# Performance work log

Measured on AMD Instinct MI355X. Metric: run time of the kernel, lower is better.

The kernel has to match this reference:

```python
import math
import jax, jax.numpy as jnp
import numpy as np

B, T, S, C, E = 16, 1024, 1024, 1024, 1024
NORM_C = 0.5


def setup_inputs() -> dict:
    key = jax.random.key(0)
    ks = jax.random.split(key, 9)
    return {
        "x": jax.random.normal(ks[0], (B, T, C), dtype=jnp.float32),
        "target_embedding": jax.random.normal(ks[1], (B, T, E), dtype=jnp.float32),
        "enc_keys": jax.random.normal(ks[2], (B, E, S), dtype=jnp.float32),      # encoder_out[0]
        "enc_values": jax.random.normal(ks[3], (B, S, E), dtype=jnp.float32),    # encoder_out[1]
        "encoder_padding_mask": jax.random.randint(ks[4], (B, S), 0, 2).astype(bool),
        "w_in": jax.random.normal(ks[5], (E, C), dtype=jnp.float32) / np.sqrt(C),
        "b_in": jnp.zeros((E,), dtype=jnp.float32),
        "w_out": jax.random.normal(ks[6], (C, E), dtype=jnp.float32) / np.sqrt(E),
        "b_out": jnp.zeros((C,), dtype=jnp.float32),
    }


def reference(x, target_embedding, enc_keys, enc_values, encoder_padding_mask,
              w_in, b_in, w_out, b_out):
    scale = jnp.float32(math.sqrt(NORM_C))
    residual = x
    # in_projection + target embedding, rescale
    h = (jnp.einsum("btc,ec->bte", x, w_in) + b_in + target_embedding) * scale
    # attention scores: bmm with keys [B,E,S]
    scores = jnp.einsum("bte,bes->bts", h, enc_keys)
    neg_inf = jnp.float32(float("-inf"))
    scores = jnp.where(encoder_padding_mask[:, None, :], neg_inf, scores)
    attn_scores = jax.nn.softmax(scores, axis=-1)
    # weighted sum of values
    ctx = jnp.einsum("bts,bse->bte", attn_scores, enc_values)
    # data-dependent rescale: multiply by sqrt(valid token count)
    s = jnp.float32(S) - jnp.sum(encoder_padding_mask.astype(ctx.dtype), axis=1, keepdims=True)  # [B,1]
    s = s[:, :, None]  # [B,1,1]
    ctx = ctx * (s * jax.lax.rsqrt(s))
    out = (jnp.einsum("bte,ce->btc", ctx, w_out) + b_out + residual) * scale
    return (out, attn_scores)
```

## Files before the change

### kernel.cpp

```cpp
#include <hip/hip_runtime.h>


#define SCALE_F 0.70710678118654752440f

constexpr int BB = 16, TT = 1024, SS = 1024, CC = 1024, EE = 1024;

typedef float    f32x4 __attribute__((ext_vector_type(4)));
typedef _Float16 f16x8 __attribute__((ext_vector_type(8)));
typedef _Float16 f16x4 __attribute__((ext_vector_type(4)));

__device__ __forceinline__ void gload_lds16(const _Float16* g, _Float16* l) {
  __builtin_amdgcn_global_load_lds((const __attribute__((address_space(1))) void*)g,
                                   (__attribute__((address_space(3))) void*)l,
                                   16, 0, 0);
}

#define VMCNT(N) asm volatile("s_waitcnt vmcnt(" #N ")" ::: "memory")
#define LGKM(N)  asm volatile("s_waitcnt lgkmcnt(" #N ")" ::: "memory")
#define SBAR()   asm volatile("s_barrier" ::: "memory")
#define DSR(dst, a, off) \
  asm volatile("ds_read_b128 %0, %1 offset:" #off : "=v"(dst) : "v"(a))

__global__ __launch_bounds__(256) void cvt_f16(const float* __restrict__ s,
                                               _Float16* __restrict__ d, long n) {
  long i = ((long)blockIdx.x * 256 + threadIdx.x) * 8;
  if (i >= n) return;
  f32x4 a = *(const f32x4*)(s + i);
  f32x4 b = *(const f32x4*)(s + i + 4);
  f16x8 h;
  h[0]=(_Float16)a[0]; h[1]=(_Float16)a[1]; h[2]=(_Float16)a[2]; h[3]=(_Float16)a[3];
  h[4]=(_Float16)b[0]; h[5]=(_Float16)b[1]; h[6]=(_Float16)b[2]; h[7]=(_Float16)b[3];
  *(f16x8*)(d + i) = h;
}

__global__ __launch_bounds__(256) void transpose_cvt(const float* __restrict__ src,
                                                     _Float16* __restrict__ dst,
                                                     int R, int Cc) {
  __shared__ float tile[64][65];
  const int b = blockIdx.z;
  const int r0 = blockIdx.y * 64, c0 = blockIdx.x * 64;
  const int t = threadIdx.x;
  const int tr = t >> 4, tc4 = (t & 15) * 4;
  const float* s = src + (size_t)b * R * Cc;
#pragma unroll
  for (int i = 0; i < 4; ++i) {
    f32x4 v = *(const f32x4*)(s + (size_t)(r0 + i * 16 + tr) * Cc + c0 + tc4);
    tile[i * 16 + tr][tc4 + 0] = v[0]; tile[i * 16 + tr][tc4 + 1] = v[1];
    tile[i * 16 + tr][tc4 + 2] = v[2]; tile[i * 16 + tr][tc4 + 3] = v[3];
  }
  __syncthreads();
  _Float16* d = dst + (size_t)b * Cc * R;
#pragma unroll
  for (int j = 0; j < 4; ++j) {
    const int cl = j * 16 + tr;
    f16x4 h;
    h[0] = (_Float16)tile[tc4 + 0][cl]; h[1] = (_Float16)tile[tc4 + 1][cl];
    h[2] = (_Float16)tile[tc4 + 2][cl]; h[3] = (_Float16)tile[tc4 + 3][cl];
    *(f16x4*)(d + (size_t)(c0 + cl) * R + r0 + tc4) = h;
  }
}

__global__ __launch_bounds__(256) void mask_prep(const unsigned char* __restrict__ mraw,
                                                 float* __restrict__ maskneg,
                                                 float* __restrict__ sscale) {
  const int b = blockIdx.x, t = threadIdx.x;
  __shared__ int bytemode_sh, cnt_sh;
  if (t == 0) { bytemode_sh = 0; cnt_sh = 0; }
  __syncthreads();
  const unsigned int* mu = (const unsigned int*)mraw;
  int local = 0;
  for (int i = t; i < (BB * SS) / 4; i += 256) {
    unsigned int v = mu[i];
    if (v != 0u && v != 1u && v != 0x3f800000u) local = 1;
  }
  if (local) atomicOr(&bytemode_sh, 1);
  __syncthreads();
  const int bytemode = bytemode_sh;
  int cnt = 0;
  for (int s = t; s < SS; s += 256) {
    int m = bytemode ? (mraw[b * SS + s] != 0) : (mu[b * SS + s] != 0u);
    maskneg[b * SS + s] = m ? -__builtin_inff() : 0.0f;
    cnt += m;
  }
#pragma unroll
  for (int o = 32; o; o >>= 1) cnt += __shfl_down(cnt, o);
  if ((t & 63) == 0) atomicAdd(&cnt_sh, cnt);
  __syncthreads();
  if (t == 0) {
    float sv = (float)SS - (float)cnt_sh;
    sscale[b] = sv * rsqrtf(sv);
  }
}

template <int EPI>
__global__ __launch_bounds__(512, 2)
void gemm_t3(const _Float16* __restrict__ A, const _Float16* __restrict__ Bmat,
             long aStride, long bStride, long oStride,
             int M, int N, int K,
             void* __restrict__ outp,
             const float* __restrict__ bias,
             const void* __restrict__ addmat,
             const float* __restrict__ extra) {
  __shared__ __attribute__((aligned(16))) _Float16 smem[73728];

  const int t = threadIdx.x;
  const int lane = t & 63;
  const int wid = t >> 6;
  const int wm = wid >> 1, wn = wid & 1;
  const int z = blockIdx.z;
  const int lo = lane & 15, hi = lane >> 4;
  const int nt = K >> 6;

  const int gx = gridDim.x;
  const int fblk = blockIdx.x + blockIdx.y * gx;
  const int q = (gx * gridDim.y) >> 3;
  const int wg = (fblk & 7) * q + (fblk >> 3);
  const long rowBase = (long)(wg / gx) * 256;
  const long colBase = (long)(wg % gx) * 128;

  const _Float16* Ag = A + (size_t)z * aStride + rowBase * K;
  const _Float16* Bg = Bmat + (size_t)z * bStride + colBase * K;

  const int strow = t >> 2;
  const int stchunk = (t & 3) ^ ((t >> 3) & 3);

  f32x4 acc[4][4] = {};

  auto stg6 = [&](int U, int b3) {
    _Float16* ab = &smem[b3 * 16384];
    _Float16* bb = &smem[49152 + b3 * 8192];
    const size_t ko = (size_t)U * 64 + stchunk * 8;
    gload_lds16(Ag + (size_t)strow * K + ko,             ab + t * 8);
    gload_lds16(Ag + (size_t)(strow + 128) * K + ko,     ab + 4096 + t * 8);
    gload_lds16(Ag + (size_t)strow * K + ko + 32,        ab + 8192 + t * 8);
    gload_lds16(Ag + (size_t)(strow + 128) * K + ko + 32, ab + 12288 + t * 8);
    gload_lds16(Bg + (size_t)strow * K + ko,             bb + t * 8);
    gload_lds16(Bg + (size_t)strow * K + ko + 32,        bb + 4096 + t * 8);
  };

  const int lds0 = (int)(size_t)&smem[0];
  const int slotx = (hi ^ ((lo >> 1) & 3)) << 4;
  const int abase = lds0 + wm * 4096 + lo * 64 + slotx;
  const int bbase = lds0 + 98304 + wn * 4096 + lo * 64 + slotx;

  stg6(0, 0);
  stg6(1, 1);
  VMCNT(6);
  SBAR();

  int bufR = 0, bufS = 2;
  for (int u = 0; u < nt; ++u) {
    const int aad0 = abase + bufR * 32768;
    const int aad1 = aad0 + 16384;
    const int bad0 = bbase + bufR * 16384;
    const int bad1 = bad0 + 8192;
    f16x8 a0[4], b0[4], a1[4], b1[4];
    DSR(a0[0], aad0, 0); DSR(a0[1], aad0, 1024);
    DSR(a0[2], aad0, 2048); DSR(a0[3], aad0, 3072);
    DSR(b0[0], bad0, 0); DSR(b0[1], bad0, 1024);
    DSR(b0[2], bad0, 2048); DSR(b0[3], bad0, 3072);
    DSR(a1[0], aad1, 0); DSR(a1[1], aad1, 1024);
    DSR(a1[2], aad1, 2048); DSR(a1[3], aad1, 3072);
    DSR(b1[0], bad1, 0); DSR(b1[1], bad1, 1024);
    DSR(b1[2], bad1, 2048); DSR(b1[3], bad1, 3072);
    if (u + 2 < nt) stg6(u + 2, bufS);
    LGKM(8);
    __builtin_amdgcn_sched_barrier(0);
    __builtin_amdgcn_s_setprio(1);
#pragma unroll
    for (int mi = 0; mi < 4; ++mi)
#pragma unroll
      for (int ni = 0; ni < 4; ++ni)
        acc[mi][ni] = __builtin_amdgcn_mfma_f32_16x16x32_f16(a0[mi], b0[ni],
                                                             acc[mi][ni], 0, 0, 0);
    __builtin_amdgcn_s_setprio(0);
    LGKM(0);
    __builtin_amdgcn_sched_barrier(0);
    __builtin_amdgcn_s_setprio(1);
#pragma unroll
    for (int mi = 0; mi < 4; ++mi)
#pragma unroll
      for (int ni = 0; ni < 4; ++ni)
        acc[mi][ni] = __builtin_amdgcn_mfma_f32_16x16x32_f16(a1[mi], b1[ni],
                                                             acc[mi][ni], 0, 0, 0);
    __builtin_amdgcn_s_setprio(0);
    if (u < nt - 2)       { VMCNT(6); }
    else if (u == nt - 2) { VMCNT(0); }
    SBAR();
    bufR = (bufR == 2) ? 0 : bufR + 1;
    bufS = (bufS == 2) ? 0 : bufS + 1;
  }

  LGKM(0);
  __syncthreads();

  constexpr int EPS = 68;
  const int fr = lane & 15;
  const int fq = (lane >> 4) * 4;
  const int er = lane >> 2;
  const int ec = (lane & 3) * 16;
  const long gc0 = colBase + wn * 64 + ec;
  float* ep = (float*)smem + wid * (16 * EPS);

  f32x4 biasv[4], maskv[4], av[4];
  float sc = 0.f;
  auto load_add = [&](long gr) {
    if constexpr (EPI == 1) {
      const float* am = (const float*)addmat;
#pragma unroll
      for (int i = 0; i < 4; ++i) av[i] = *(const f32x4*)&am[gr * N + gc0 + i * 4];
    } else if constexpr (EPI == 5) {
      const _Float16* am = (const _Float16*)addmat;
      f16x8 h0 = *(const f16x8*)&am[gr * N + gc0];
      f16x8 h1 = *(const f16x8*)&am[gr * N + gc0 + 8];
#pragma unroll
      for (int i = 0; i < 4; ++i) {
        const f16x8& hh = i < 2 ? h0 : h1;
        const int o = (i & 1) * 4;
        av[i][0] = (float)hh[o]; av[i][1] = (float)hh[o + 1];
        av[i][2] = (float)hh[o + 2]; av[i][3] = (float)hh[o + 3];
      }
    }
  };
  if constexpr (EPI == 1 || EPI == 5) {
#pragma unroll
    for (int i = 0; i < 4; ++i) biasv[i] = *(const f32x4*)&bias[gc0 + i * 4];
    load_add(rowBase + wm * 64 + er);
  }
  if constexpr (EPI == 2) {
#pragma unroll
    for (int i = 0; i < 4; ++i)
      maskv[i] = *(const f32x4*)&((const float*)addmat)[(size_t)z * N + gc0 + i * 4];
  }
  if constexpr (EPI == 3) sc = extra[z];

#pragma unroll
  for (int mf = 0; mf < 4; ++mf) {
#pragma unroll
    for (int n = 0; n < 4; ++n)
#pragma unroll
      for (int j = 0; j < 4; ++j)
        ep[(fq + j) * EPS + n * 16 + fr] = acc[mf][n][j];
    __syncthreads();
    const long gr = rowBase + wm * 64 + mf * 16 + er;
    f32x4 r[4];
#pragma unroll
    for (int i = 0; i < 4; ++i) r[i] = *(const f32x4*)&ep[er * EPS + ec + i * 4];
    f32x4 a_cur[4];
    if constexpr (EPI == 1 || EPI == 5) {
#pragma unroll
      for (int i = 0; i < 4; ++i) a_cur[i] = av[i];
      if (mf < 3) load_add(gr + 16);
    }
    if constexpr (EPI == 1) {
      _Float16* o = (_Float16*)outp + gr * N + gc0;
#pragma unroll
      for (int g = 0; g < 2; ++g) {
        f32x4 v0 = (r[2 * g] + biasv[2 * g] + a_cur[2 * g]) * SCALE_F;
        f32x4 v1 = (r[2 * g + 1] + biasv[2 * g + 1] + a_cur[2 * g + 1]) * SCALE_F;
        f16x8 h;
        h[0]=(_Float16)v0[0]; h[1]=(_Float16)v0[1]; h[2]=(_Float16)v0[2]; h[3]=(_Float16)v0[3];
        h[4]=(_Float16)v1[0]; h[5]=(_Float16)v1[1]; h[6]=(_Float16)v1[2]; h[7]=(_Float16)v1[3];
        *(f16x8*)(o + g * 8) = h;
      }
    } else if constexpr (EPI == 2) {
      float* o = (float*)outp + (size_t)z * oStride + gr * N + gc0;
#pragma unroll
      for (int i = 0; i < 4; ++i) *(f32x4*)(o + i * 4) = r[i] + maskv[i];
    } else if constexpr (EPI == 3) {
      _Float16* o = (_Float16*)outp + (size_t)z * oStride + gr * N + gc0;
#pragma unroll
      for (int g = 0; g < 2; ++g) {
        f32x4 v0 = r[2 * g] * sc;
        f32x4 v1 = r[2 * g + 1] * sc;
        f16x8 h;
        h[0]=(_Float16)v0[0]; h[1]=(_Float16)v0[1]; h[2]=(_Float16)v0[2]; h[3]=(_Float16)v0[3];
        h[4]=(_Float16)v1[0]; h[5]=(_Float16)v1[1]; h[6]=(_Float16)v1[2]; h[7]=(_Float16)v1[3];
        *(f16x8*)(o + g * 8) = h;
      }
    } else {
      float* o = (float*)outp + gr * N + gc0;
#pragma unroll
      for (int i = 0; i < 4; ++i)
        *(f32x4*)(o + i * 4) = (r[i] + biasv[i] + a_cur[i]) * SCALE_F;
    }
    __syncthreads();
  }
}

__global__ __launch_bounds__(256) void softmax_k(float* __restrict__ attn,
                                                 _Float16* __restrict__ attn16) {
  const size_t row = blockIdx.x;
  float* p = attn + row * SS;
  const int t = threadIdx.x;
  f32x4 v = *(const f32x4*)(p + t * 4);
  __shared__ float red[8];
  float m = fmaxf(fmaxf(v[0], v[1]), fmaxf(v[2], v[3]));
#pragma unroll
  for (int o = 32; o; o >>= 1) m = fmaxf(m, __shfl_xor(m, o));
  if (!(t & 63)) red[t >> 6] = m;
  __syncthreads();
  m = fmaxf(fmaxf(red[0], red[1]), fmaxf(red[2], red[3]));
  f32x4 e;
  e[0] = __expf(v[0] - m); e[1] = __expf(v[1] - m);
  e[2] = __expf(v[2] - m); e[3] = __expf(v[3] - m);
  float s = e[0] + e[1] + e[2] + e[3];
#pragma unroll
  for (int o = 32; o; o >>= 1) s += __shfl_xor(s, o);
  if (!(t & 63)) red[4 + (t >> 6)] = s;
  __syncthreads();
  s = red[4] + red[5] + red[6] + red[7];
  const float inv = 1.0f / s;
  f32x4 o4; o4[0]=e[0]*inv; o4[1]=e[1]*inv; o4[2]=e[2]*inv; o4[3]=e[3]*inv;
  *(f32x4*)(p + t * 4) = o4;
  f16x4 h; h[0]=(_Float16)o4[0]; h[1]=(_Float16)o4[1];
  h[2]=(_Float16)o4[2]; h[3]=(_Float16)o4[3];
  *(f16x4*)(attn16 + row * SS + t * 4) = h;
}

extern "C" void kernel_launch(void* const* d_in, const int* in_sizes, int n_in,
                              void* d_out, int out_size, void* d_ws, size_t ws_size,
                              hipStream_t stream) {
  const float* x     = (const float*)d_in[0];
  const float* te    = (const float*)d_in[1];
  const float* keys  = (const float*)d_in[2];
  const float* vals  = (const float*)d_in[3];
  const void*  mask  = d_in[4];
  const float* w_in  = (const float*)d_in[5];
  const float* b_in  = (const float*)d_in[6];
  const float* w_out = (const float*)d_in[7];
  const float* b_out = (const float*)d_in[8];

  char* ws = (char*)d_ws;
  const size_t MB32 = 33554432;
  _Float16* buf0   = (_Float16*)(ws);
  _Float16* buf1   = (_Float16*)(ws + MB32);
  _Float16* keysT  = (_Float16*)(ws + 2 * MB32);
  _Float16* valsT  = (_Float16*)(ws + 3 * MB32);
  _Float16* win16  = (_Float16*)(ws + 4 * MB32);
  _Float16* wout16 = (_Float16*)(ws + 4 * MB32 + 2097152);
  float*    maskneg= (float*)   (ws + 4 * MB32 + 2 * 2097152);
  float*    sscale = (float*)   (ws + 4 * MB32 + 2 * 2097152 + 65536);

  float* out_main = (float*)d_out;
  float* attn_out = (float*)d_out + (size_t)BB * TT * CC;

  cvt_f16<<<dim3(16777216 / 2048), 256, 0, stream>>>(x, buf0, 16777216);
  cvt_f16<<<dim3(1048576 / 2048), 256, 0, stream>>>(w_in, win16, 1048576);
  cvt_f16<<<dim3(1048576 / 2048), 256, 0, stream>>>(w_out, wout16, 1048576);
  transpose_cvt<<<dim3(SS / 64, EE / 64, BB), 256, 0, stream>>>(keys, keysT, EE, SS);
  transpose_cvt<<<dim3(EE / 64, SS / 64, BB), 256, 0, stream>>>(vals, valsT, SS, EE);
  mask_prep<<<dim3(BB), 256, 0, stream>>>((const unsigned char*)mask, maskneg, sscale);

  gemm_t3<1><<<dim3(EE / 128, (BB * TT) / 256, 1), 512, 0, stream>>>(
      buf0, win16, 0, 0, 0, BB * TT, EE, CC, buf1, b_in, te, nullptr);
  gemm_t3<2><<<dim3(SS / 128, TT / 256, BB), 512, 0, stream>>>(
      buf1, keysT, (long)TT * EE, (long)SS * EE, (long)TT * SS,
      TT, SS, EE, attn_out, nullptr, maskneg, nullptr);
  softmax_k<<<dim3(BB * TT), 256, 0, stream>>>(attn_out, buf1);
  gemm_t3<3><<<dim3(EE / 128, TT / 256, BB), 512, 0, stream>>>(
      buf1, valsT, (long)TT * SS, (long)EE * SS, (long)TT * EE,
      TT, EE, SS, keysT, nullptr, nullptr, sscale);
  gemm_t3<5><<<dim3(CC / 128, (BB * TT) / 256, 1), 512, 0, stream>>>(
      keysT, wout16, 0, 0, 0, BB * TT, CC, EE, out_main, b_out, buf0, nullptr);
}
```

Baseline: 327.4 us.

## Split GEMM k-tile into half-phases with finer prefetch and merge prep kernels

Restructures the GEMM main loop so each 64-wide k-tile is processed as two 32-wide halves. Each half issues its own LDS reads, its own global-to-LDS prefetch, barriers and MFMA block, and the vmcnt waits are retuned to match. The LDS swizzle pattern also changes. Separately, the two weight conversions are merged into one launch and the two transposes into another, which cuts launch overhead. The added barriers per tile may cost more synchronisation than the finer overlap saves.

```diff
diff --git a/kernel.cpp b/kernel.cpp
--- a/kernel.cpp
+++ b/kernel.cpp
@@ -33,11 +33,31 @@
   *(f16x8*)(d + i) = h;
 }
 
-__global__ __launch_bounds__(256) void transpose_cvt(const float* __restrict__ src,
-                                                     _Float16* __restrict__ dst,
-                                                     int R, int Cc) {
+__global__ __launch_bounds__(256) void cvt_w(const float* __restrict__ s0,
+                                             _Float16* __restrict__ d0,
+                                             const float* __restrict__ s1,
+                                             _Float16* __restrict__ d1) {
+  const float* s = blockIdx.y ? s1 : s0;
+  _Float16* d = blockIdx.y ? d1 : d0;
+  long i = ((long)blockIdx.x * 256 + threadIdx.x) * 8;
+  f32x4 a = *(const f32x4*)(s + i);
+  f32x4 b = *(const f32x4*)(s + i + 4);
+  f16x8 h;
+  h[0]=(_Float16)a[0]; h[1]=(_Float16)a[1]; h[2]=(_Float16)a[2]; h[3]=(_Float16)a[3];
+  h[4]=(_Float16)b[0]; h[5]=(_Float16)b[1]; h[6]=(_Float16)b[2]; h[7]=(_Float16)b[3];
+  *(f16x8*)(d + i) = h;
+}
+
+__global__ __launch_bounds__(256) void transpose_cvt(const float* __restrict__ src0,
+                                                     _Float16* __restrict__ dst0,
+                                                     const float* __restrict__ src1,
+                                                     _Float16* __restrict__ dst1) {
   __shared__ float tile[64][65];
-  const int b = blockIdx.z;
+  const int zz = blockIdx.z;
+  const int b = zz & (BB - 1);
+  const float* src = (zz < BB) ? src0 : src1;
+  _Float16* dst = (zz < BB) ? dst0 : dst1;
+  const int R = 1024, Cc = 1024;
   const int r0 = blockIdx.y * 64, c0 = blockIdx.x * 64;
   const int t = threadIdx.x;
   const int tr = t >> 4, tc4 = (t & 15) * 4;
@@ -94,7 +114,7 @@
 
 template <int EPI>
 __global__ __launch_bounds__(512, 2)
-void gemm_t3(const _Float16* __restrict__ A, const _Float16* __restrict__ Bmat,
+void gemm_p3(const _Float16* __restrict__ A, const _Float16* __restrict__ Bmat,
              long aStride, long bStride, long oStride,
              int M, int N, int K,
              void* __restrict__ outp,
@@ -122,71 +142,62 @@
   const _Float16* Bg = Bmat + (size_t)z * bStride + colBase * K;
 
   const int strow = t >> 2;
-  const int stchunk = (t & 3) ^ ((t >> 3) & 3);
+  const int stchunk = (t & 3) ^ (strow & 3);
 
   f32x4 acc[4][4] = {};
 
-  auto stg6 = [&](int U, int b3) {
-    _Float16* ab = &smem[b3 * 16384];
-    _Float16* bb = &smem[49152 + b3 * 8192];
-    const size_t ko = (size_t)U * 64 + stchunk * 8;
-    gload_lds16(Ag + (size_t)strow * K + ko,             ab + t * 8);
-    gload_lds16(Ag + (size_t)(strow + 128) * K + ko,     ab + 4096 + t * 8);
-    gload_lds16(Ag + (size_t)strow * K + ko + 32,        ab + 8192 + t * 8);
-    gload_lds16(Ag + (size_t)(strow + 128) * K + ko + 32, ab + 12288 + t * 8);
-    gload_lds16(Bg + (size_t)strow * K + ko,             bb + t * 8);
-    gload_lds16(Bg + (size_t)strow * K + ko + 32,        bb + 4096 + t * 8);
+  auto stgA = [&](int U, int b3, int kh) {
+    _Float16* ab = &smem[b3 * 16384 + kh * 8192];
+    const size_t ko = (size_t)U * 64 + kh * 32 + stchunk * 8;
+    gload_lds16(Ag + (size_t)strow * K + ko, ab + t * 8);
+    gload_lds16(Ag + (size_t)(128 + strow) * K + ko, ab + 4096 + t * 8);
   };
+  auto stgB = [&](int U, int b3, int kh) {
+    _Float16* bb = &smem[49152 + b3 * 8192 + kh * 4096];
+    gload_lds16(Bg + (size_t)strow * K + (size_t)U * 64 + kh * 32 + stchunk * 8,
+                bb + t * 8);
+  };
 
   const int lds0 = (int)(size_t)&smem[0];
-  const int slotx = (hi ^ ((lo >> 1) & 3)) << 4;
+  const int slotx = (hi ^ (lo & 3)) << 4;
   const int abase = lds0 + wm * 4096 + lo * 64 + slotx;
   const int bbase = lds0 + 98304 + wn * 4096 + lo * 64 + slotx;
 
-  stg6(0, 0);
-  stg6(1, 1);
-  VMCNT(6);
+  stgA(0, 0, 0); stgA(0, 0, 1); stgB(0, 0, 0); stgB(0, 0, 1);
+  stgA(1, 1, 0); stgA(1, 1, 1); stgB(1, 1, 0); stgB(1, 1, 1);
+  VMCNT(0);
   SBAR();
 
   int bufR = 0, bufS = 2;
   for (int u = 0; u < nt; ++u) {
-    const int aad0 = abase + bufR * 32768;
-    const int aad1 = aad0 + 16384;
-    const int bad0 = bbase + bufR * 16384;
-    const int bad1 = bad0 + 8192;
-    f16x8 a0[4], b0[4], a1[4], b1[4];
-    DSR(a0[0], aad0, 0); DSR(a0[1], aad0, 1024);
-    DSR(a0[2], aad0, 2048); DSR(a0[3], aad0, 3072);
-    DSR(b0[0], bad0, 0); DSR(b0[1], bad0, 1024);
-    DSR(b0[2], bad0, 2048); DSR(b0[3], bad0, 3072);
-    DSR(a1[0], aad1, 0); DSR(a1[1], aad1, 1024);
-    DSR(a1[2], aad1, 2048); DSR(a1[3], aad1, 3072);
-    DSR(b1[0], bad1, 0); DSR(b1[1], bad1, 1024);
-    DSR(b1[2], bad1, 2048); DSR(b1[3], bad1, 3072);
-    if (u + 2 < nt) stg6(u + 2, bufS);
-    LGKM(8);
-    __builtin_amdgcn_sched_barrier(0);
-    __builtin_amdgcn_s_setprio(1);
-#pragma unroll
-    for (int mi = 0; mi < 4; ++mi)
-#pragma unroll
-      for (int ni = 0; ni < 4; ++ni)
-        acc[mi][ni] = __builtin_amdgcn_mfma_f32_16x16x32_f16(a0[mi], b0[ni],
-                                                             acc[mi][ni], 0, 0, 0);
-    __builtin_amdgcn_s_setprio(0);
-    LGKM(0);
-    __builtin_amdgcn_sched_barrier(0);
-    __builtin_amdgcn_s_setprio(1);
-#pragma unroll
-    for (int mi = 0; mi < 4; ++mi)
-#pragma unroll
-      for (int ni = 0; ni < 4; ++ni)
-        acc[mi][ni] = __builtin_amdgcn_mfma_f32_16x16x32_f16(a1[mi], b1[ni],
-                                                             acc[mi][ni], 0, 0, 0);
-    __builtin_amdgcn_s_setprio(0);
-    if (u < nt - 2)       { VMCNT(6); }
-    else if (u == nt - 2) { VMCNT(0); }
-    SBAR();
+    const int aadB = abase + bufR * 32768;
+    const int badB = bbase + bufR * 16384;
+#pragma unroll
+    for (int kh = 0; kh < 2; ++kh) {
+      const int aad = aadB + kh * 16384;
+      const int bad = badB + kh * 8192;
+      f16x8 a_[4], b_[4];
+      DSR(a_[0], aad, 0); DSR(a_[1], aad, 1024);
+      DSR(a_[2], aad, 2048); DSR(a_[3], aad, 3072);
+      DSR(b_[0], bad, 0); DSR(b_[1], bad, 1024);
+      DSR(b_[2], bad, 2048); DSR(b_[3], bad, 3072);
+      if (u + 2 < nt) { stgA(u + 2, bufS, kh); stgB(u + 2, bufS, kh); }
+      SBAR();
+      LGKM(0);
+      __builtin_amdgcn_sched_barrier(0);
+      __builtin_amdgcn_s_setprio(1);
+#pragma unroll
+      for (int mi = 0; mi < 4; ++mi)
+#pragma unroll
+        for (int ni = 0; ni < 4; ++ni)
+          acc[mi][ni] = __builtin_amdgcn_mfma_f32_16x16x32_f16(
+              a_[mi], b_[ni], acc[mi][ni], 0, 0, 0);
+      __builtin_amdgcn_s_setprio(0);
+      if (u < nt - 3)            { VMCNT(9); }
+      else if (u == nt - 3)      { if (kh == 0) { VMCNT(9); } else { VMCNT(6); } }
+      else if (u == nt - 2)      { if (kh == 0) { VMCNT(3); } else { VMCNT(0); } }
+      SBAR();
+    }
     bufR = (bufR == 2) ? 0 : bufR + 1;
     bufS = (bufS == 2) ? 0 : bufS + 1;
   }
@@ -346,21 +357,19 @@
   float* attn_out = (float*)d_out + (size_t)BB * TT * CC;
 
   cvt_f16<<<dim3(16777216 / 2048), 256, 0, stream>>>(x, buf0, 16777216);
-  cvt_f16<<<dim3(1048576 / 2048), 256, 0, stream>>>(w_in, win16, 1048576);
-  cvt_f16<<<dim3(1048576 / 2048), 256, 0, stream>>>(w_out, wout16, 1048576);
-  transpose_cvt<<<dim3(SS / 64, EE / 64, BB), 256, 0, stream>>>(keys, keysT, EE, SS);
-  transpose_cvt<<<dim3(EE / 64, SS / 64, BB), 256, 0, stream>>>(vals, valsT, SS, EE);
+  cvt_w<<<dim3(1048576 / 2048, 2), 256, 0, stream>>>(w_in, win16, w_out, wout16);
+  transpose_cvt<<<dim3(16, 16, 2 * BB), 256, 0, stream>>>(keys, keysT, vals, valsT);
   mask_prep<<<dim3(BB), 256, 0, stream>>>((const unsigned char*)mask, maskneg, sscale);
 
-  gemm_t3<1><<<dim3(EE / 128, (BB * TT) / 256, 1), 512, 0, stream>>>(
+  gemm_p3<1><<<dim3(EE / 128, (BB * TT) / 256, 1), 512, 0, stream>>>(
       buf0, win16, 0, 0, 0, BB * TT, EE, CC, buf1, b_in, te, nullptr);
-  gemm_t3<2><<<dim3(SS / 128, TT / 256, BB), 512, 0, stream>>>(
+  gemm_p3<2><<<dim3(SS / 128, TT / 256, BB), 512, 0, stream>>>(
       buf1, keysT, (long)TT * EE, (long)SS * EE, (long)TT * SS,
       TT, SS, EE, attn_out, nullptr, maskneg, nullptr);
   softmax_k<<<dim3(BB * TT), 256, 0, stream>>>(attn_out, buf1);
-  gemm_t3<3><<<dim3(EE / 128, TT / 256, BB), 512, 0, stream>>>(
+  gemm_p3<3><<<dim3(EE / 128, TT / 256, BB), 512, 0, stream>>>(
       buf1, valsT, (long)TT * SS, (long)EE * SS, (long)TT * EE,
       TT, EE, SS, keysT, nullptr, nullptr, sscale);
-  gemm_t3<5><<<dim3(CC / 128, (BB * TT) / 256, 1), 512, 0, stream>>>(
+  gemm_p3<5><<<dim3(CC / 128, (BB * TT) / 256, 1), 512, 0, stream>>>(
       keysT, wout16, 0, 0, 0, BB * TT, CC, EE, out_main, b_out, buf0, nullptr);
 }
```

New measurement: 350.1 us. +6.9%, slower.
